# Kernel tuning notes

Hardware: AMD Instinct MI355X
Metric: run time of the kernel (lower is better)

Reference implementation:

```python
import jax, jax.numpy as jnp
import numpy as np

B, S, DIM = 4, 1024, 2048
N_HEAD, N_KV, HEAD_DIM = 32, 8, 64


def setup_inputs() -> dict:
    key = jax.random.key(0)
    k1, k2, k3, k4 = jax.random.split(key, 4)
    x = jax.random.normal(k1, (B, S, DIM), dtype=jnp.float32)
    # rotary table: [S, head_dim//2, 2] = (cos, sin)
    inv_freq = 1.0 / (10000.0 ** (jnp.arange(0, HEAD_DIM, 2, dtype=jnp.float32) / HEAD_DIM))
    t = jnp.arange(S, dtype=jnp.float32)
    ang = t[:, None] * inv_freq[None, :]
    freqs_cis = jnp.stack([jnp.cos(ang), jnp.sin(ang)], axis=-1)
    mask = jnp.tril(jnp.ones((S, S), dtype=bool))[None, None]  # causal bool [1,1,S,S]
    scale = 0.02
    wqkv = jax.random.normal(k2, ((N_HEAD + 2 * N_KV) * HEAD_DIM, DIM), dtype=jnp.float32) * scale
    wo = jax.random.normal(k3, (DIM, DIM), dtype=jnp.float32) * scale
    return {"x": x, "freqs_cis": freqs_cis, "mask": mask, "wqkv": wqkv, "wo": wo}


def _apply_rotary(x, freqs_cis):
    # x: [b, s, h, d]; freqs_cis: [s, d//2, 2]
    b, s, h, d = x.shape
    xr = x.reshape(b, s, h, d // 2, 2)
    fc = freqs_cis.reshape(1, s, 1, d // 2, 2)
    cos, sin = fc[..., 0], fc[..., 1]
    x0, x1 = xr[..., 0], xr[..., 1]
    out = jnp.stack([x0 * cos - x1 * sin, x1 * cos + x0 * sin], axis=-1)
    return out.reshape(b, s, h, d)


def reference(x, freqs_cis, mask, wqkv, wo):
    b, s, _ = x.shape
    qkv = jnp.einsum('bsd,ed->bse', x, wqkv)
    q, k, v = jnp.split(qkv, [N_HEAD * HEAD_DIM, (N_HEAD + N_KV) * HEAD_DIM], axis=-1)
    q = q.reshape(b, s, N_HEAD, HEAD_DIM)
    k = k.reshape(b, s, N_KV, HEAD_DIM)
    v = v.reshape(b, s, N_KV, HEAD_DIM)
    q = _apply_rotary(q, freqs_cis)
    k = _apply_rotary(k, freqs_cis)
    # [b, h, s, d]
    q = q.transpose(0, 2, 1, 3)
    k = k.transpose(0, 2, 1, 3)
    v = v.transpose(0, 2, 1, 3)
    g = N_HEAD // N_KV
    k = jnp.repeat(k, g, axis=1)
    v = jnp.repeat(v, g, axis=1)
    scale = 1.0 / np.sqrt(HEAD_DIM).astype(np.float32)
    scores = jnp.einsum('bhqd,bhkd->bhqk', q, k) * scale
    scores = jnp.where(mask, scores, jnp.float32(-jnp.inf))
    attn = jax.nn.softmax(scores, axis=-1)
    y = jnp.einsum('bhqk,bhkd->bhqd', attn, v)
    y = y.transpose(0, 2, 1, 3).reshape(b, s, DIM)
    return jnp.einsum('bsd,ed->bse', y, wo)
```

## Files before the change

kernel.cpp:

```cpp
#include <hip/hip_runtime.h>
#include <stdint.h>

typedef __bf16 bf16;
typedef __attribute__((ext_vector_type(8))) __bf16 bf16x8;
typedef __attribute__((ext_vector_type(4))) __bf16 bf16x4;
typedef __attribute__((ext_vector_type(4))) float f32x4;
typedef __attribute__((ext_vector_type(16))) float f32x16;
typedef __attribute__((ext_vector_type(2))) unsigned u32x2;

#define AS1 __attribute__((address_space(1)))
#define AS3 __attribute__((address_space(3)))

#if __has_builtin(__builtin_amdgcn_permlane32_swap)
#define HAVE_PLSWAP 1
#else
#define HAVE_PLSWAP 0
#endif

__device__ __forceinline__ float ex2(float x) {
#if __has_builtin(__builtin_amdgcn_exp2f)
  return __builtin_amdgcn_exp2f(x);
#else
  return exp2f(x);
#endif
}

__device__ __forceinline__ void barrier_f() {
  asm volatile("" ::: "memory");
  __builtin_amdgcn_s_barrier();
  asm volatile("" ::: "memory");
}

template <int N>
__device__ __forceinline__ void waitVm() {
  if constexpr (N == 0) asm volatile("s_waitcnt vmcnt(0)" ::: "memory");
  else if constexpr (N == 1) asm volatile("s_waitcnt vmcnt(1)" ::: "memory");
  else if constexpr (N == 2) asm volatile("s_waitcnt vmcnt(2)" ::: "memory");
  else if constexpr (N == 4) asm volatile("s_waitcnt vmcnt(4)" ::: "memory");
  else if constexpr (N == 6) asm volatile("s_waitcnt vmcnt(6)" ::: "memory");
  else if constexpr (N == 8) asm volatile("s_waitcnt vmcnt(8)" ::: "memory");
  else static_assert(N == 0, "unsupported vmcnt");
  __builtin_amdgcn_sched_barrier(0);
}

__device__ __forceinline__ u32x2 swap32(uint32_t a, uint32_t b, int hh) {
#if HAVE_PLSWAP
  (void)hh;
  return __builtin_amdgcn_permlane32_swap(a, b, false, false);
#else
  u32x2 r;
  r[0] = hh ? __shfl_xor(b, 32) : a;
  r[1] = hh ? b : __shfl_xor(a, 32);
  return r;
#endif
}

template <int K>
__device__ __forceinline__ void relay_body(const float* __restrict__ W,
                                           bf16* __restrict__ Bp, int t) {
  const int off = t * 8;
  const int sub = (off & 511) >> 3;
  const int n = sub & 15, khi = sub >> 4;
  const int blk = off >> 9;
  const int kblk = blk & ((K >> 5) - 1);
  const int nblk = blk >> (31 - __builtin_clz(K >> 5));
  const float* src = W + (size_t)(nblk * 16 + n) * K + kblk * 32 + khi * 8;
  float4 a = *reinterpret_cast<const float4*>(src);
  float4 b = *reinterpret_cast<const float4*>(src + 4);
  bf16x8 o = { (bf16)a.x, (bf16)a.y, (bf16)a.z, (bf16)a.w,
               (bf16)b.x, (bf16)b.y, (bf16)b.z, (bf16)b.w };
  *reinterpret_cast<bf16x8*>(Bp + off) = o;
}

__global__ __launch_bounds__(256) void prologue_kernel(
    const float* __restrict__ x, bf16* __restrict__ xb,
    const float* __restrict__ wqkv, bf16* __restrict__ BpQ) {
  const int blk = blockIdx.x;
  if (blk < 8192) {
    const int i = blk * 256 + threadIdx.x;
    float4 v = reinterpret_cast<const float4*>(x)[i];
    bf16x4 r = { (bf16)v.x, (bf16)v.y, (bf16)v.z, (bf16)v.w };
    reinterpret_cast<bf16x4*>(xb)[i] = r;
  } else {
    relay_body<2048>(wqkv, BpQ, (blk - 8192) * 256 + threadIdx.x);
  }
}

template <int BN, typename OutT, bool FUSE, int MINW>
__global__ __launch_bounds__(512, MINW) void gemmfc2(
    const bf16* __restrict__ A, const bf16* __restrict__ Bp,
    OutT* __restrict__ C, const float* __restrict__ fc,
    bf16* __restrict__ Qd, bf16* __restrict__ Kd, bf16* __restrict__ Vd,
    int N, int K) {
  constexpr int WTN = BN / 8;
  constexpr int NR = WTN / 16;
  constexpr int NBF = 2 * NR;
  constexpr int ABUF = 64 * 128;
  __shared__ char smem[2 * ABUF];
  AS3 char* sm3 = (AS3 char*)smem;

  const int tid = threadIdx.x;
  const int w = tid >> 6, lane = tid & 63;
  const int fr = lane & 15, fq = lane >> 4;
  const int xorA = (fr & 7) << 4;

  const int orig = blockIdx.x;
  const int cpx = (int)gridDim.x >> 3;
  const int wgid = (orig & 7) * cpx + (orig >> 3);
  const int bm = (wgid & 63) * 64;
  const int bn = (wgid >> 6) * BN;
  const int KB = K >> 5;
  const int nbBase = (bn >> 4) + w * NR;

  f32x4 acc[4][NR] = {};

  auto stageA = [&](int t, int buf) {
    AS3 char* db = sm3 + buf * ABUF;
    const int row = tid >> 3;
    const int kslot = (tid & 7) ^ (row & 7);
    __builtin_amdgcn_global_load_lds(
        (const AS1 void*)(A + (size_t)(bm + row) * K + t * 64 + kslot * 8),
        (AS3 void*)(db + w * 1024), 16, 0, 0);
  };

  stageA(0, 0);

  const int NT = K >> 6;
  for (int t = 0; t < NT; ++t) {
    const int cb = t & 1;
    const bool pf = (t + 1 < NT);
    bf16x8 bF[NR][2];
#pragma unroll
    for (int ni = 0; ni < NR; ++ni)
#pragma unroll
      for (int ks = 0; ks < 2; ++ks)
        bF[ni][ks] = *reinterpret_cast<const bf16x8*>(
            Bp + ((size_t)(nbBase + ni) * KB + t * 2 + ks) * 512 + lane * 8);
    waitVm<NBF>();
    barrier_f();
    if (pf) stageA(t + 1, cb ^ 1);
    const char* cbA = smem + cb * ABUF;
    bf16x8 aF[2][2];
#pragma unroll
    for (int mi = 0; mi < 2; ++mi)
#pragma unroll
      for (int ks = 0; ks < 2; ++ks)
        aF[mi][ks] = *reinterpret_cast<const bf16x8*>(
            cbA + (mi * 16 + fr) * 128 + ((ks * 64 + fq * 16) ^ xorA));
    if (pf) waitVm<1>(); else waitVm<0>();
#pragma unroll
    for (int mp = 0; mp < 2; ++mp) {
      if (mp > 0) {
#pragma unroll
        for (int mi = 0; mi < 2; ++mi)
#pragma unroll
          for (int ks = 0; ks < 2; ++ks)
            aF[mi][ks] = *reinterpret_cast<const bf16x8*>(
                cbA + (32 + mi * 16 + fr) * 128 + ((ks * 64 + fq * 16) ^ xorA));
      }
      __builtin_amdgcn_s_setprio(1);
#pragma unroll
      for (int ks = 0; ks < 2; ++ks)
#pragma unroll
        for (int mi = 0; mi < 2; ++mi)
#pragma unroll
          for (int ni = 0; ni < NR; ++ni)
            acc[mp * 2 + mi][ni] = __builtin_amdgcn_mfma_f32_16x16x32_bf16(
                aF[mi][ks], bF[ni][ks], acc[mp * 2 + mi][ni], 0, 0, 0);
      __builtin_amdgcn_s_setprio(0);
    }
  }

  if constexpr (FUSE) {
    barrier_f();
    float* smF = (float*)smem;
    {
      const float* fsrc = fc + (size_t)(bm & 1023) * 64;
#pragma unroll
      for (int k = 0; k < 2; ++k)
        reinterpret_cast<float4*>(smF)[tid + k * 512] =
            reinterpret_cast<const float4*>(fsrc)[tid + k * 512];
    }
    __syncthreads();
    const float QSCALE = 0.125f * 1.4426950408889634f;
    const int par = fr & 1;
#pragma unroll
    for (int ni = 0; ni < NR; ++ni) {
      const int col = bn + w * WTN + ni * 16 + fr;
#pragma unroll
      for (int mi = 0; mi < 4; ++mi) {
        const int sl = mi * 16 + fq * 4;
        const int row0 = bm + sl;
        const int bb = row0 >> 10, s0 = row0 & 1023;
        if (col < 2560) {
          const int e = (col < 2048) ? col : col - 2048;
          const int d = e & 63, hq = e >> 6;
          const int dbase = d & ~1;
          bf16* dst = (col < 2048)
              ? Qd + (((size_t)(bb * 32 + hq)) * 1024 + s0) * 64 + d
              : Kd + (((size_t)(bb * 8 + hq)) * 1024 + s0) * 64 + d;
#pragma unroll
          for (int j = 0; j < 4; ++j) {
            float v = acc[mi][ni][j];
            float pv = __shfl_xor(v, 1);
            float2 csn = *reinterpret_cast<const float2*>(
                &smF[(sl + j) * 64 + dbase]);
            float r = par ? (v * csn.x + pv * csn.y)
                          : (v * csn.x - pv * csn.y);
            if (col < 2048) r *= QSCALE;
            dst[(size_t)j * 64] = (bf16)r;
          }
        } else {
          const int e = col - 2560, d = e & 63, hv = e >> 6;
          bf16x4 pk4;
#pragma unroll
          for (int j = 0; j < 4; ++j) pk4[j] = (bf16)acc[mi][ni][j];
          *reinterpret_cast<bf16x4*>(
              Vd + (((size_t)(bb * 8 + hv)) * 64 + d) * 1024 + s0) = pk4;
        }
      }
    }
  } else {
    const int cbn = bn + w * WTN + fr;
#pragma unroll
    for (int mi = 0; mi < 4; ++mi) {
      const int rb = bm + mi * 16 + fq * 4;
#pragma unroll
      for (int ni = 0; ni < NR; ++ni)
#pragma unroll
        for (int j = 0; j < 4; ++j)
          C[(size_t)(rb + j) * N + cbn + ni * 16] = (OutT)acc[mi][ni][j];
    }
  }
}

__global__ __launch_bounds__(256, 4) void attn_kernel(const bf16* __restrict__ Q,
                                                      const bf16* __restrict__ K,
                                                      const bf16* __restrict__ Vt,
                                                      bf16* __restrict__ Y,
                                                      const float* __restrict__ woSrc,
                                                      bf16* __restrict__ BpOd) {
  __shared__ bf16 smem[25600];
  char* sb = (char*)smem;
  AS3 char* sA = (AS3 char*)smem;

  const int fid = blockIdx.x;

  {
    const int tbase = fid * 1024 + (int)threadIdx.x * 4;
#pragma unroll
    for (int k = 0; k < 4; ++k)
      relay_body<2048>(woSrc, BpOd, tbase + k);
  }

  const int hkv = fid & 7;
  const int hl = (fid >> 3) & 3;
  const int b = (fid >> 5) & 3;
  const int j = (fid >> 7) & 3;
  const int h = hkv * 4 + hl;

  const int w = threadIdx.x >> 6, lane = threadIdx.x & 63;
  const int qn = lane & 31;
  const int hh = lane >> 5;
  const int srow = lane >> 3;
  const int scb = (((lane & 7) ^ srow) << 4);
  const int xsw = (qn & 7) << 4;

  const bf16* Qh = Q + ((size_t)(b * 32 + h)) * 65536;
  const char* kB = (const char*)(K + ((size_t)(b * 8 + hkv)) * 65536);
  const char* vB = (const char*)(Vt + ((size_t)(b * 8 + hkv)) * 65536);

  const int nchA = 2 * j + 2;
  const int TOT = 18;

  auto stage = [&](int ci, int buf) {
    const int kc = ci << 6;
    const int bo = buf * 8192;
#pragma unroll
    for (int i = 0; i < 2; ++i) {
      const int row = i * 32 + 8 * w + srow;
      __builtin_amdgcn_global_load_lds(
          (const AS1 void*)(kB + (size_t)(kc + row) * 128 + scb),
          (AS3 void*)(sA + bo + i * 4096 + w * 1024), 16, 0, 0);
      __builtin_amdgcn_global_load_lds(
          (const AS1 void*)(vB + (size_t)row * 2048 + kc * 2 + scb),
          (AS3 void*)(sA + 16384 + bo + i * 4096 + w * 1024), 16, 0, 0);
    }
  };

  auto applyMask = [&](f32x16* st, int kc, int qg) {
#pragma unroll
    for (int mt = 0; mt < 2; ++mt)
#pragma unroll
      for (int r = 0; r < 16; ++r) {
        int kv = kc + mt * 32 + (r & 3) + 8 * (r >> 2) + 4 * hh;
        if (kv > qg) st[mt][r] = -3e38f;
      }
  };

  union F32U { float f; uint32_t u; };
  union W64 { uint32_t u; bf16 b[2]; };

  int tq0 = j * 128 + w * 32;
  int maskFrom = tq0 >> 6;
  bf16x8 qf[4];
#pragma unroll
  for (int s = 0; s < 4; ++s)
    qf[s] = *reinterpret_cast<const bf16x8*>(
        &Qh[(size_t)(tq0 + qn) * 64 + s * 16 + hh * 8]);
  f32x16 O[2] = {};
  float mrow = -3e38f, lrow = 0.f;

  auto epilogue = [&]() {
    float inv = 1.f / lrow;
    bf16* Ytw = smem + 16384 + w * 2304;
#pragma unroll
    for (int dt = 0; dt < 2; ++dt)
#pragma unroll
      for (int r = 0; r < 16; ++r) {
        int d = dt * 32 + (r & 3) + 8 * (r >> 2) + 4 * hh;
        Ytw[qn * 72 + d] = (bf16)(O[dt][r] * inv);
      }
    asm volatile("s_waitcnt lgkmcnt(0)" ::: "memory");
    const int qr = lane >> 1, c0 = (lane & 1) * 32;
    bf16* yout = Y + ((size_t)(b * 1024 + tq0 - w * 32 + (w * 32) + qr)) * 2048 + h * 64 + c0;
#pragma unroll
    for (int i = 0; i < 4; ++i)
      *reinterpret_cast<bf16x8*>(&yout[i * 8]) =
          *reinterpret_cast<const bf16x8*>(&Ytw[qr * 72 + c0 + i * 8]);
  };

  stage(0, 0);

  for (int s = 0; s < TOT; ++s) {
    const int cur = s & 1;
    const int c = (s < nchA) ? s : s - nchA;
    if (s + 1 < TOT) {
      stage((s + 1 < nchA) ? s + 1 : s + 1 - nchA, cur ^ 1);
      waitVm<4>();
    } else {
      waitVm<0>();
    }
    barrier_f();
    const int kc = c << 6;
    const char* Kc = sb + cur * 8192;
    const char* Vc = sb + 16384 + cur * 8192;

    bf16x8 kf[2][4];
#pragma unroll
    for (int mt = 0; mt < 2; ++mt)
#pragma unroll
      for (int si = 0; si < 4; ++si)
        kf[mt][si] = *reinterpret_cast<const bf16x8*>(
            Kc + (qn + 32 * mt) * 128 + ((32 * si + 16 * hh) ^ xsw));
    f32x16 st[2] = {};
#pragma unroll
    for (int mt = 0; mt < 2; ++mt)
#pragma unroll
      for (int si = 0; si < 4; ++si)
        st[mt] = __builtin_amdgcn_mfma_f32_32x32x16_bf16(kf[mt][si], qf[si], st[mt], 0, 0, 0);
    if (c >= maskFrom) applyMask(st, kc, tq0 + qn);
    float t16[16];
#pragma unroll
    for (int i = 0; i < 16; ++i) t16[i] = fmaxf(st[0][i], st[1][i]);
#pragma unroll
    for (int off = 8; off >= 1; off >>= 1)
#pragma unroll
      for (int i = 0; i < off; ++i) t16[i] = fmaxf(t16[i], t16[i + off]);
    F32U fm; fm.f = t16[0];
    u32x2 rm = swap32(fm.u, fm.u, hh);
    F32U m0, m1; m0.u = rm[0]; m1.u = rm[1];
    float mx = fmaxf(m0.f, m1.f);
    if (!__all(mx - mrow <= 8.f)) {
      float mnew = fmaxf(mrow, mx);
      float alpha = ex2(mrow - mnew);
      lrow *= alpha;
#pragma unroll
      for (int dt = 0; dt < 2; ++dt)
#pragma unroll
        for (int r = 0; r < 16; ++r) O[dt][r] *= alpha;
      mrow = mnew;
    }
    W64 pk[2][8];
    float ps[16];
#pragma unroll
    for (int t = 0; t < 2; ++t)
#pragma unroll
      for (int wi = 0; wi < 8; ++wi) {
        float p0 = ex2(st[t][2 * wi] - mrow);
        float p1 = ex2(st[t][2 * wi + 1] - mrow);
        ps[t * 8 + wi] = p0 + p1;
        pk[t][wi].b[0] = (bf16)p0;
        pk[t][wi].b[1] = (bf16)p1;
      }
#pragma unroll
    for (int off = 8; off >= 1; off >>= 1)
#pragma unroll
      for (int i = 0; i < off; ++i) ps[i] += ps[i + off];
    F32U fs; fs.f = ps[0];
    u32x2 rs = swap32(fs.u, fs.u, hh);
    F32U s0, s1; s0.u = rs[0]; s1.u = rs[1];
    lrow += s0.f + s1.f;
#pragma unroll
    for (int si = 0; si < 4; ++si) {
      const int t = si >> 1, a0 = 4 * (si & 1);
      u32x2 rA = swap32(pk[t][a0 + 0].u, pk[t][a0 + 2].u, hh);
      u32x2 rB = swap32(pk[t][a0 + 1].u, pk[t][a0 + 3].u, hh);
      union BF { uint32_t u[4]; bf16x8 v; } bfrag;
      bfrag.u[0] = rA[0];
      bfrag.u[1] = rB[0];
      bfrag.u[2] = rA[1];
      bfrag.u[3] = rB[1];
#pragma unroll
      for (int dt = 0; dt < 2; ++dt) {
        bf16x8 vf = *reinterpret_cast<const bf16x8*>(
            Vc + (qn + 32 * dt) * 128 + ((32 * si + 16 * hh) ^ xsw));
        O[dt] = __builtin_amdgcn_mfma_f32_32x32x16_bf16(vf, bfrag.v, O[dt], 0, 0, 0);
      }
    }
    barrier_f();

    if (s == nchA - 1) {
      const int nq0 = (7 - j) * 128 + w * 32;
      bf16x8 nqf[4];
#pragma unroll
      for (int si = 0; si < 4; ++si)
        nqf[si] = *reinterpret_cast<const bf16x8*>(
            &Qh[(size_t)(nq0 + qn) * 64 + si * 16 + hh * 8]);
      epilogue();
      tq0 = nq0;
      maskFrom = tq0 >> 6;
#pragma unroll
      for (int si = 0; si < 4; ++si) qf[si] = nqf[si];
#pragma unroll
      for (int dt = 0; dt < 2; ++dt)
#pragma unroll
        for (int r = 0; r < 16; ++r) O[dt][r] = 0.f;
      mrow = -3e38f;
      lrow = 0.f;
    }
  }

  epilogue();
}

extern "C" void kernel_launch(void* const* d_in, const int* in_sizes, int n_in,
                              void* d_out, int out_size, void* d_ws, size_t ws_size,
                              hipStream_t stream) {
  const float* x    = (const float*)d_in[0];
  const float* fc   = (const float*)d_in[1];
  const float* wqkv = (const float*)d_in[3];
  const float* wo   = (const float*)d_in[4];
  float* out = (float*)d_out;

  char* ws = (char*)d_ws;
  const size_t MB = 1u << 20;
  bf16* xb    = (bf16*)(ws);
  bf16* BpQ   = (bf16*)(ws + 16 * MB);
  bf16* BpO   = (bf16*)(ws + 28 * MB);
  bf16* Qr    = (bf16*)(ws + 60 * MB);
  bf16* Kr    = (bf16*)(ws + 76 * MB);
  bf16* Vt    = (bf16*)(ws + 80 * MB);
  bf16* Y     = (bf16*)(ws + 84 * MB);

  prologue_kernel<<<11264, 256, 0, stream>>>(x, xb, wqkv, BpQ);

  gemmfc2<384, bf16, true, 4><<<512, 512, 0, stream>>>(
      xb, BpQ, (bf16*)nullptr, fc, Qr, Kr, Vt, 3072, 2048);

  attn_kernel<<<512, 256, 0, stream>>>(Qr, Kr, Vt, Y, wo, BpO);

  gemmfc2<128, float, false, 8><<<1024, 512, 0, stream>>>(
      Y, BpO, out, nullptr, nullptr, nullptr, nullptr, 2048, 2048);
}
```

Measured before the change: 153.9 us.

## Replace output projection GEMM with dedicated 128x64 tile kernel reading B fragments directly

Adds a specialized kernel for the output projection that stages only A tiles (128 rows × 64 k) in LDS via global_load_lds double buffering. It loads pre-packed B fragments straight from global memory into registers, and each wave computes a 16×64 output strip with MFMA 16x16x32. The change is meant to cut LDS traffic for B and simplify the loop compared with the generic gemmfc2 path. In exchange, B fragments are reloaded from global/L2 by every workgroup, which adds memory pressure. Each wave also holds a small accumulator, which lowers the compute per load.

```diff
diff --git a/kernel.cpp b/kernel.cpp
--- a/kernel.cpp
+++ b/kernel.cpp
@@ -234,6 +234,84 @@
   }
 }
 
+__global__ __launch_bounds__(512, 2) void gemm_wo_mrow(
+    const bf16* __restrict__ A, const bf16* __restrict__ Bp,
+    float* __restrict__ C, int N, int K) {
+  constexpr int ABUF = 128 * 128;
+  __shared__ char smem[2 * ABUF];
+  AS3 char* sm3 = (AS3 char*)smem;
+
+  const int tid = threadIdx.x;
+  const int w = tid >> 6, lane = tid & 63;
+  const int fr = lane & 15, fq = lane >> 4;
+  const int xorA = (fr & 7) << 4;
+
+  const int orig = blockIdx.x;
+  const int cpx = (int)gridDim.x >> 3;
+  const int wgid = (orig & 7) * cpx + (orig >> 3);
+  const int bm = (wgid & 31) * 128;
+  const int bn = (wgid >> 5) * 64;
+  const int KB = K >> 5;
+  const int nbBase = bn >> 4;
+
+  f32x4 acc[4] = {};
+
+  auto stageA = [&](int t, int buf) {
+    AS3 char* db = sm3 + buf * ABUF;
+    const int r0 = tid >> 3;
+    const int kslot = (tid & 7) ^ (r0 & 7);
+#pragma unroll
+    for (int i = 0; i < 2; ++i) {
+      const int row = i * 64 + r0;
+      __builtin_amdgcn_global_load_lds(
+          (const AS1 void*)(A + (size_t)(bm + row) * K + t * 64 + kslot * 8),
+          (AS3 void*)(db + i * 8192 + w * 1024), 16, 0, 0);
+    }
+  };
+
+  stageA(0, 0);
+
+  const int NT = K >> 6;
+  for (int t = 0; t < NT; ++t) {
+    const int cb = t & 1;
+    const bool pf = (t + 1 < NT);
+    bf16x8 bF[4][2];
+#pragma unroll
+    for (int ni = 0; ni < 4; ++ni)
+#pragma unroll
+      for (int ks = 0; ks < 2; ++ks)
+        bF[ni][ks] = *reinterpret_cast<const bf16x8*>(
+            Bp + ((size_t)(nbBase + ni) * KB + t * 2 + ks) * 512 + lane * 8);
+    waitVm<8>();
+    barrier_f();
+    if (pf) stageA(t + 1, cb ^ 1);
+    const char* cbA = smem + cb * ABUF;
+    bf16x8 aF[2];
+#pragma unroll
+    for (int ks = 0; ks < 2; ++ks)
+      aF[ks] = *reinterpret_cast<const bf16x8*>(
+          cbA + (w * 16 + fr) * 128 + ((ks * 64 + fq * 16) ^ xorA));
+    if (pf) waitVm<2>(); else waitVm<0>();
+    __builtin_amdgcn_s_setprio(1);
+#pragma unroll
+    for (int ks = 0; ks < 2; ++ks)
+#pragma unroll
+      for (int ni = 0; ni < 4; ++ni)
+        acc[ni] = __builtin_amdgcn_mfma_f32_16x16x32_bf16(
+            aF[ks], bF[ni][ks], acc[ni], 0, 0, 0);
+    __builtin_amdgcn_s_setprio(0);
+  }
+
+  const int rb = bm + w * 16 + fq * 4;
+#pragma unroll
+  for (int ni = 0; ni < 4; ++ni) {
+    const int col = bn + ni * 16 + fr;
+#pragma unroll
+    for (int j = 0; j < 4; ++j)
+      C[(size_t)(rb + j) * N + col] = acc[ni][j];
+  }
+}
+
 __global__ __launch_bounds__(256, 4) void attn_kernel(const bf16* __restrict__ Q,
                                                       const bf16* __restrict__ K,
                                                       const bf16* __restrict__ Vt,
@@ -470,6 +548,5 @@
 
   attn_kernel<<<512, 256, 0, stream>>>(Qr, Kr, Vt, Y, wo, BpO);
 
-  gemmfc2<128, float, false, 8><<<1024, 512, 0, stream>>>(
-      Y, BpO, out, nullptr, nullptr, nullptr, nullptr, 2048, 2048);
-}
+  gemm_wo_mrow<<<1024, 512, 0, stream>>>(Y, BpO, out, 2048, 2048);
+}
```

New measurement: 198.0 us. 28.6% more time.
